# Kernel tuning notes

Measured on AMD Instinct MI355X. Metric: run time of the kernel, lower is better.

## Reference

```python
import jax, jax.numpy as jnp
import numpy as np

DIM = 1024


def _combine(e1, e2):
    # associative op for h_t = a_t * h_{t-1} + b_t (inclusive scan, h_0-contrib handled outside)
    a1, b1 = e1
    a2, b2 = e2
    return a1 * a2, b2 + a2 * b1


def setup_inputs() -> dict:
    key = jax.random.key(0)
    ks = jax.random.split(key, 11)
    s = 1.0 / np.sqrt(DIM)
    d = {
        "x": jax.random.normal(ks[0], (4, 4096, DIM), jnp.float32),
        "hidden": jax.random.normal(ks[1], (4, DIM), jnp.float32),
        "Wf": jax.random.uniform(ks[2], (DIM, DIM), jnp.float32, -s, s),
        "bf": jax.random.uniform(ks[3], (DIM,), jnp.float32, -s, s),
        "Wi": jax.random.uniform(ks[4], (DIM, DIM), jnp.float32, -s, s),
        "bi": jax.random.uniform(ks[5], (DIM,), jnp.float32, -s, s),
        "Wig": jax.random.uniform(ks[6], (DIM, DIM), jnp.float32, -s, s),
        "big": jax.random.uniform(ks[7], (DIM,), jnp.float32, -s, s),
        "Wog": jax.random.uniform(ks[8], (DIM, DIM), jnp.float32, -s, s),
        "bog": jax.random.uniform(ks[9], (DIM,), jnp.float32, -s, s),
    }
    return d


def reference(x, hidden, Wf, bf, Wi, bi, Wig, big, Wog, bog):
    # x: [B, L, D], hidden: [B, D]
    forget = jax.nn.sigmoid(jnp.einsum("bld,ed->ble", x, Wf) + bf)
    inp = jnp.tanh(jnp.einsum("bld,ed->ble", x, Wi) + bi) * \
          jax.nn.sigmoid(jnp.einsum("bld,ed->ble", x, Wig) + big)
    # parallel scan of h_t = forget_t * h_{t-1} + inp_t with h_0 = 0
    _, h_inner = jax.lax.associative_scan(_combine, (forget, inp), axis=1)
    # add initial-hidden contribution: hidden * prod_{s<=t} forget_s
    h = h_inner + hidden[:, None, :] * jnp.cumprod(forget, axis=1)
    y = jnp.tanh(h) * jax.nn.sigmoid(jnp.einsum("bld,ed->ble", x, Wog) + bog)
    return y, h[:, -1, :]
```

## Files before the change

### kernel.cpp

```cpp
#include <hip/hip_runtime.h>
#include <hip/hip_bf16.h>
#include <cstdint>
#include <cstddef>

#define DIMD 1024
#define LSEQ 4096
#define BATCH 4
#define MTOT (BATCH*LSEQ)
#define NCHUNK 64
#define CHUNKLEN 64
#define GATE_ELEMS ((size_t)MTOT*DIMD)
#define NTILE_K 16

typedef __bf16 bf16x8 __attribute__((ext_vector_type(8)));
typedef float f32x4 __attribute__((ext_vector_type(4)));

__device__ __forceinline__ unsigned short f2bf(float f) {
    union { float f; uint32_t u; } v; v.f = f;
    uint32_t r = v.u + 0x7fffu + ((v.u >> 16) & 1u);
    return (unsigned short)(r >> 16);
}
__device__ __forceinline__ float bits2f(unsigned short b) {
    union { uint32_t u; float f; } v; v.u = ((uint32_t)b) << 16; return v.f;
}
__device__ __forceinline__ float gld(const float* p, size_t o) { return p[o]; }
__device__ __forceinline__ float gld(const unsigned short* p, size_t o) { return bits2f(p[o]); }
__device__ __forceinline__ void  gst(float* p, size_t o, float v) { p[o] = v; }
__device__ __forceinline__ void  gst(unsigned short* p, size_t o, float v) { p[o] = f2bf(v); }

__device__ __forceinline__ float fsig(float x) {
    return __builtin_amdgcn_rcpf(1.f + __expf(-x));
}

__global__ void cast_f32_to_bf16(const float* __restrict__ src,
                                 unsigned short* __restrict__ dst, int n) {
    int i = (blockIdx.x * blockDim.x + threadIdx.x) * 8;
    if (i >= n) return;
    float4 a = *(const float4*)(src + i);
    float4 b = *(const float4*)(src + i + 4);
    uint4 o;
    o.x = (uint32_t)f2bf(a.x) | ((uint32_t)f2bf(a.y) << 16);
    o.y = (uint32_t)f2bf(a.z) | ((uint32_t)f2bf(a.w) << 16);
    o.z = (uint32_t)f2bf(b.x) | ((uint32_t)f2bf(b.y) << 16);
    o.w = (uint32_t)f2bf(b.z) | ((uint32_t)f2bf(b.w) << 16);
    *(uint4*)(dst + i) = o;
}

template <typename T>
__global__ __launch_bounds__(512, 1) void gemm_gates8(
    const unsigned short* __restrict__ Xb,
    const unsigned short* __restrict__ Wcat,
    const float* __restrict__ bf_, const float* __restrict__ bi_,
    const float* __restrict__ big_, const float* __restrict__ bog_,
    T* __restrict__ G)
{
    __shared__ __align__(16) char lds[131072];
    char* ldsA = lds;
    char* ldsB = lds + 65536;

    const int tid = threadIdx.x;
    const int wave = tid >> 6, lane = tid & 63;
    const int wm = wave >> 2, wn = wave & 3;
    const int l15 = lane & 15, l4 = lane >> 4;

    const int wg = blockIdx.x;
    const int swz = (wg & 7) * 128 + (wg >> 3);
    const int mt = swz & 63, nt = swz >> 6;
    const int m0 = mt * 256, n0 = nt * 256;

    auto stage = [&](const unsigned short* src, int rowbase, int k0, char* region, int buf) {
#pragma unroll
        for (int half = 0; half < 2; ++half) {
            char* slot = region + (buf * 2 + half) * 16384;
#pragma unroll
            for (int j = 0; j < 2; ++j) {
                int r = (tid >> 3) + j * 64;
                int scol = (tid & 7) ^ (r & 7);
                const unsigned short* g = src + (size_t)(rowbase + half * 128 + r) * DIMD + k0 + scol * 8;
                __builtin_amdgcn_global_load_lds(
                    (const __attribute__((address_space(1))) uint32_t*)g,
                    (__attribute__((address_space(3))) uint32_t*)(slot + (wave << 10) + (j << 13)),
                    16, 0, 0);
            }
        }
    };

    f32x4 acc[8][4];
#pragma unroll
    for (int m = 0; m < 8; ++m)
#pragma unroll
        for (int n = 0; n < 4; ++n) acc[m][n] = (f32x4)0.f;

    stage(Xb, m0, 0, ldsA, 0);   stage(Wcat, n0, 0, ldsB, 0);
    stage(Xb, m0, 64, ldsA, 1);  stage(Wcat, n0, 64, ldsB, 1);

#pragma unroll 1
    for (int t = 0; t < NTILE_K; ++t) {
        const int buf = t & 1;
        if (t == NTILE_K - 1) asm volatile("s_waitcnt vmcnt(0)" ::: "memory");
        else                  asm volatile("s_waitcnt vmcnt(8)" ::: "memory");
        __builtin_amdgcn_s_barrier();

        const char* Aslot = ldsA + (buf * 2 + wm) * 16384;
        const char* Bslot = ldsB + (buf * 2 + (wn >> 1)) * 16384;
        const int rbB = (wn & 1) * 64;

        auto rdA = [&](int mq, int i, int kk) -> bf16x8 {
            int r = (mq * 4 + i) * 16 + l15;
            int s = kk * 4 + l4;
            return *(const bf16x8*)(Aslot + r * 128 + ((s ^ (r & 7)) << 4));
        };
        auto rdB = [&](int nq, int i2, int kk) -> bf16x8 {
            int r = rbB + (nq * 2 + i2) * 16 + l15;
            int s = kk * 4 + l4;
            return *(const bf16x8*)(Bslot + r * 128 + ((s ^ (r & 7)) << 4));
        };

        bf16x8 av0[4][2], av1[4][2], bv0[2][2], bv1[2][2];
#pragma unroll
        for (int i = 0; i < 4; ++i)
#pragma unroll
            for (int kk = 0; kk < 2; ++kk) av0[i][kk] = rdA(0, i, kk);
#pragma unroll
        for (int i2 = 0; i2 < 2; ++i2)
#pragma unroll
            for (int kk = 0; kk < 2; ++kk) { bv0[i2][kk] = rdB(0, i2, kk); bv1[i2][kk] = rdB(1, i2, kk); }

        __builtin_amdgcn_s_setprio(1);
#pragma unroll
        for (int kk = 0; kk < 2; ++kk)
#pragma unroll
            for (int i = 0; i < 4; ++i)
#pragma unroll
                for (int i2 = 0; i2 < 2; ++i2)
                    acc[i][i2] = __builtin_amdgcn_mfma_f32_16x16x32_bf16(av0[i][kk], bv0[i2][kk], acc[i][i2], 0, 0, 0);
        __builtin_amdgcn_s_setprio(0);

#pragma unroll
        for (int i = 0; i < 4; ++i)
#pragma unroll
            for (int kk = 0; kk < 2; ++kk) av1[i][kk] = rdA(1, i, kk);

        __builtin_amdgcn_s_setprio(1);
#pragma unroll
        for (int kk = 0; kk < 2; ++kk)
#pragma unroll
            for (int i = 0; i < 4; ++i)
#pragma unroll
                for (int i2 = 0; i2 < 2; ++i2)
                    acc[i][2 + i2] = __builtin_amdgcn_mfma_f32_16x16x32_bf16(av0[i][kk], bv1[i2][kk], acc[i][2 + i2], 0, 0, 0);
        __builtin_amdgcn_s_setprio(0);

        __builtin_amdgcn_s_setprio(1);
#pragma unroll
        for (int kk = 0; kk < 2; ++kk)
#pragma unroll
            for (int i = 0; i < 4; ++i)
#pragma unroll
                for (int i2 = 0; i2 < 2; ++i2)
                    acc[4 + i][i2] = __builtin_amdgcn_mfma_f32_16x16x32_bf16(av1[i][kk], bv0[i2][kk], acc[4 + i][i2], 0, 0, 0);
        __builtin_amdgcn_s_setprio(0);

        __builtin_amdgcn_s_setprio(1);
#pragma unroll
        for (int kk = 0; kk < 2; ++kk)
#pragma unroll
            for (int i = 0; i < 4; ++i)
#pragma unroll
                for (int i2 = 0; i2 < 2; ++i2)
                    acc[4 + i][2 + i2] = __builtin_amdgcn_mfma_f32_16x16x32_bf16(av1[i][kk], bv1[i2][kk], acc[4 + i][2 + i2], 0, 0, 0);
        __builtin_amdgcn_s_setprio(0);

        __builtin_amdgcn_s_barrier();
        if (t + 2 < NTILE_K) {
            stage(Xb, m0, (t + 2) * 64, ldsA, buf);
            stage(Wcat, n0, (t + 2) * 64, ldsB, buf);
        }
    }

    const int gate = n0 >> 10;
    const float* bias = (gate == 0) ? bf_ : (gate == 1) ? bi_ : (gate == 2) ? big_ : bog_;
    T* Gg = G + (size_t)gate * GATE_ELEMS;
    const int ebase = (n0 & 1023) + wn * 64;
    const int rowb0 = m0 + wm * 128;
    float bvv[4];
#pragma unroll
    for (int nf = 0; nf < 4; ++nf) bvv[nf] = bias[ebase + nf * 16 + l15];
#pragma unroll
    for (int mf = 0; mf < 8; ++mf) {
        int rowb = rowb0 + mf * 16 + l4 * 4;
#pragma unroll
        for (int r = 0; r < 4; ++r) {
            size_t rowoff = (size_t)(rowb + r) * DIMD;
#pragma unroll
            for (int nf = 0; nf < 4; ++nf) {
                float pre = acc[mf][nf][r] + bvv[nf];
                float v = (gate == 1) ? (2.f * fsig(2.f * pre) - 1.f) : fsig(pre);
                gst(Gg, rowoff + ebase + nf * 16 + l15, v);
            }
        }
    }
}

template <typename T>
__global__ void scan_phase1(const T* __restrict__ F, const T* __restrict__ TI,
                            const T* __restrict__ SG,
                            float* __restrict__ Aagg, float* __restrict__ Bagg) {
    const int d = blockIdx.x * blockDim.x + threadIdx.x;
    const int c = blockIdx.y, b = blockIdx.z;
    size_t base = ((size_t)b * LSEQ + (size_t)c * CHUNKLEN) * DIMD + d;
    float A = 1.f, Bv = 0.f;
#pragma unroll 8
    for (int t = 0; t < CHUNKLEN; ++t) {
        size_t off = base + (size_t)t * DIMD;
        float f = gld(F, off);
        float i = gld(TI, off) * gld(SG, off);
        A *= f;
        Bv = __builtin_fmaf(f, Bv, i);
    }
    size_t o = ((size_t)b * NCHUNK + c) * DIMD + d;
    Aagg[o] = A;
    Bagg[o] = Bv;
}

__global__ void scan_phase2(const float* __restrict__ Aagg, const float* __restrict__ Bagg,
                            const float* __restrict__ hidden,
                            float* __restrict__ Hstart, float* __restrict__ out_h) {
    int idx = blockIdx.x * blockDim.x + threadIdx.x;
    int b = idx >> 10, d = idx & 1023;
    float h = hidden[b * 1024 + d];
    for (int c = 0; c < NCHUNK; ++c) {
        size_t o = ((size_t)b * NCHUNK + c) * DIMD + d;
        Hstart[o] = h;
        h = __builtin_fmaf(Aagg[o], h, Bagg[o]);
    }
    out_h[b * 1024 + d] = h;
}

template <typename T>
__global__ void scan_phase3(const T* __restrict__ F, const T* __restrict__ TI,
                            const T* __restrict__ SG, const T* __restrict__ OG,
                            const float* __restrict__ Hstart, float* __restrict__ y) {
    const int d = blockIdx.x * blockDim.x + threadIdx.x;
    const int c = blockIdx.y, b = blockIdx.z;
    float h = Hstart[((size_t)b * NCHUNK + c) * DIMD + d];
    size_t base = ((size_t)b * LSEQ + (size_t)c * CHUNKLEN) * DIMD + d;
#pragma unroll 4
    for (int t = 0; t < CHUNKLEN; ++t) {
        size_t off = base + (size_t)t * DIMD;
        float f = gld(F, off);
        float i = gld(TI, off) * gld(SG, off);
        h = __builtin_fmaf(f, h, i);
        y[off] = tanhf(h) * gld(OG, off);
    }
}

extern "C" void kernel_launch(void* const* d_in, const int* in_sizes, int n_in,
                              void* d_out, int out_size, void* d_ws, size_t ws_size,
                              hipStream_t stream) {
    const float* x      = (const float*)d_in[0];
    const float* hidden = (const float*)d_in[1];
    const float* Wf  = (const float*)d_in[2];
    const float* bf_ = (const float*)d_in[3];
    const float* Wi  = (const float*)d_in[4];
    const float* bi_ = (const float*)d_in[5];
    const float* Wig = (const float*)d_in[6];
    const float* big_= (const float*)d_in[7];
    const float* Wog = (const float*)d_in[8];
    const float* bog_= (const float*)d_in[9];

    char* ws = (char*)d_ws;
    unsigned short* Xb   = (unsigned short*)(ws);
    unsigned short* Wcat = (unsigned short*)(ws + 33554432);

    float* y     = (float*)d_out;
    float* out_h = y + GATE_ELEMS;

    cast_f32_to_bf16<<<MTOT * DIMD / 8 / 256, 256, 0, stream>>>(x, Xb, MTOT * DIMD);
    cast_f32_to_bf16<<<DIMD * DIMD / 8 / 256, 256, 0, stream>>>(Wf,  Wcat + 0 * DIMD * DIMD, DIMD * DIMD);
    cast_f32_to_bf16<<<DIMD * DIMD / 8 / 256, 256, 0, stream>>>(Wi,  Wcat + 1 * DIMD * DIMD, DIMD * DIMD);
    cast_f32_to_bf16<<<DIMD * DIMD / 8 / 256, 256, 0, stream>>>(Wig, Wcat + 2 * DIMD * DIMD, DIMD * DIMD);
    cast_f32_to_bf16<<<DIMD * DIMD / 8 / 256, 256, 0, stream>>>(Wog, Wcat + 3 * DIMD * DIMD, DIMD * DIMD);

    const size_t FP32_WS_NEED = 33554432ull + 8388608ull + GATE_ELEMS * 4 * 4 + 3ull * 1048576ull;
    if (ws_size >= FP32_WS_NEED) {
        float* G      = (float*)(ws + 41943040);
        float* Aagg   = (float*)(ws + 310378496);
        float* Bagg   = (float*)(ws + 311427072);
        float* Hstart = (float*)(ws + 312475648);
        gemm_gates8<float><<<dim3(MTOT / 256 * (4096 / 256)), 512, 0, stream>>>(
            Xb, Wcat, bf_, bi_, big_, bog_, G);
        const float* Fg  = G;
        const float* TIg = G + 1 * GATE_ELEMS;
        const float* SGg = G + 2 * GATE_ELEMS;
        const float* OGg = G + 3 * GATE_ELEMS;
        scan_phase1<float><<<dim3(DIMD / 256, NCHUNK, BATCH), 256, 0, stream>>>(Fg, TIg, SGg, Aagg, Bagg);
        scan_phase2<<<BATCH * DIMD / 256, 256, 0, stream>>>(Aagg, Bagg, hidden, Hstart, out_h);
        scan_phase3<float><<<dim3(DIMD / 256, NCHUNK, BATCH), 256, 0, stream>>>(Fg, TIg, SGg, OGg, Hstart, y);
    } else {
        unsigned short* G = (unsigned short*)(ws + 41943040);
        float* Aagg   = (float*)(ws + 176160768);
        float* Bagg   = (float*)(ws + 177209344);
        float* Hstart = (float*)(ws + 178257920);
        gemm_gates8<unsigned short><<<dim3(MTOT / 256 * (4096 / 256)), 512, 0, stream>>>(
            Xb, Wcat, bf_, bi_, big_, bog_, G);
        const unsigned short* Fg  = G;
        const unsigned short* TIg = G + 1 * GATE_ELEMS;
        const unsigned short* SGg = G + 2 * GATE_ELEMS;
        const unsigned short* OGg = G + 3 * GATE_ELEMS;
        scan_phase1<unsigned short><<<dim3(DIMD / 256, NCHUNK, BATCH), 256, 0, stream>>>(Fg, TIg, SGg, Aagg, Bagg);
        scan_phase2<<<BATCH * DIMD / 256, 256, 0, stream>>>(Aagg, Bagg, hidden, Hstart, out_h);
        scan_phase3<unsigned short><<<dim3(DIMD / 256, NCHUNK, BATCH), 256, 0, stream>>>(Fg, TIg, SGg, OGg, Hstart, y);
    }
}
```

Before: 249.6 us.

## Interleave LDS reads and next-tile prefetch between MFMA clusters in gate GEMM

Restructures the GEMM main loop into four MFMA phases separated by barriers and sched_barriers. LDS fragment reads and the global-to-LDS prefetch of tile t+2 are spread between these phases instead of sitting at the start and end of each iteration. LDS and global address computation moves out of the loop into precomputed base pointers, incremented pointers and a toggled buffer offset. The aim is to overlap memory traffic with matrix-core work and cut per-iteration address arithmetic, at the cost of extra workgroup barriers per K tile.

```diff
diff --git a/kernel.cpp b/kernel.cpp
--- a/kernel.cpp
+++ b/kernel.cpp
@@ -62,11 +62,17 @@
     const int wave = tid >> 6, lane = tid & 63;
     const int wm = wave >> 2, wn = wave & 3;
     const int l15 = lane & 15, l4 = lane >> 4;
+    const int m7 = l15 & 7;
 
     const int wg = blockIdx.x;
     const int swz = (wg & 7) * 128 + (wg >> 3);
     const int mt = swz & 63, nt = swz >> 6;
     const int m0 = mt * 256, n0 = nt * 256;
+
+    const char* Abase0 = ldsA + wm * 16384 + l15 * 128 + (((0 + l4) ^ m7) << 4);
+    const char* Abase1 = ldsA + wm * 16384 + l15 * 128 + (((4 + l4) ^ m7) << 4);
+    const char* Bbase0 = ldsB + (wn >> 1) * 16384 + ((wn & 1) * 64 + l15) * 128 + (((0 + l4) ^ m7) << 4);
+    const char* Bbase1 = ldsB + (wn >> 1) * 16384 + ((wn & 1) * 64 + l15) * 128 + (((4 + l4) ^ m7) << 4);
 
     auto stage = [&](const unsigned short* src, int rowbase, int k0, char* region, int buf) {
 #pragma unroll
@@ -85,6 +91,18 @@
         }
     };
 
+    const unsigned short* pA[2][2];
+    const unsigned short* pB[2][2];
+#pragma unroll
+    for (int half = 0; half < 2; ++half)
+#pragma unroll
+        for (int j = 0; j < 2; ++j) {
+            int r = (tid >> 3) + j * 64;
+            int scol = (tid & 7) ^ (r & 7);
+            pA[half][j] = Xb + (size_t)(m0 + half * 128 + r) * DIMD + 128 + scol * 8;
+            pB[half][j] = Wcat + (size_t)(n0 + half * 128 + r) * DIMD + 128 + scol * 8;
+        }
+
     f32x4 acc[8][4];
 #pragma unroll
     for (int m = 0; m < 8; ++m)
@@ -94,38 +112,28 @@
     stage(Xb, m0, 0, ldsA, 0);   stage(Wcat, n0, 0, ldsB, 0);
     stage(Xb, m0, 64, ldsA, 1);  stage(Wcat, n0, 64, ldsB, 1);
 
+    int bufOff = 0;
 #pragma unroll 1
     for (int t = 0; t < NTILE_K; ++t) {
-        const int buf = t & 1;
         if (t == NTILE_K - 1) asm volatile("s_waitcnt vmcnt(0)" ::: "memory");
         else                  asm volatile("s_waitcnt vmcnt(8)" ::: "memory");
         __builtin_amdgcn_s_barrier();
-
-        const char* Aslot = ldsA + (buf * 2 + wm) * 16384;
-        const char* Bslot = ldsB + (buf * 2 + (wn >> 1)) * 16384;
-        const int rbB = (wn & 1) * 64;
-
-        auto rdA = [&](int mq, int i, int kk) -> bf16x8 {
-            int r = (mq * 4 + i) * 16 + l15;
-            int s = kk * 4 + l4;
-            return *(const bf16x8*)(Aslot + r * 128 + ((s ^ (r & 7)) << 4));
-        };
-        auto rdB = [&](int nq, int i2, int kk) -> bf16x8 {
-            int r = rbB + (nq * 2 + i2) * 16 + l15;
-            int s = kk * 4 + l4;
-            return *(const bf16x8*)(Bslot + r * 128 + ((s ^ (r & 7)) << 4));
-        };
+        __builtin_amdgcn_sched_barrier(0);
 
         bf16x8 av0[4][2], av1[4][2], bv0[2][2], bv1[2][2];
-#pragma unroll
-        for (int i = 0; i < 4; ++i)
-#pragma unroll
-            for (int kk = 0; kk < 2; ++kk) av0[i][kk] = rdA(0, i, kk);
-#pragma unroll
-        for (int i2 = 0; i2 < 2; ++i2)
-#pragma unroll
-            for (int kk = 0; kk < 2; ++kk) { bv0[i2][kk] = rdB(0, i2, kk); bv1[i2][kk] = rdB(1, i2, kk); }
-
+
+#pragma unroll
+        for (int i = 0; i < 4; ++i) {
+            av0[i][0] = *(const bf16x8*)(Abase0 + bufOff + i * 2048);
+            av0[i][1] = *(const bf16x8*)(Abase1 + bufOff + i * 2048);
+        }
+#pragma unroll
+        for (int i2 = 0; i2 < 2; ++i2) {
+            bv0[i2][0] = *(const bf16x8*)(Bbase0 + bufOff + i2 * 2048);
+            bv0[i2][1] = *(const bf16x8*)(Bbase1 + bufOff + i2 * 2048);
+        }
+        __builtin_amdgcn_sched_barrier(0);
+        __builtin_amdgcn_s_barrier();
         __builtin_amdgcn_s_setprio(1);
 #pragma unroll
         for (int kk = 0; kk < 2; ++kk)
@@ -135,12 +143,16 @@
                 for (int i2 = 0; i2 < 2; ++i2)
                     acc[i][i2] = __builtin_amdgcn_mfma_f32_16x16x32_bf16(av0[i][kk], bv0[i2][kk], acc[i][i2], 0, 0, 0);
         __builtin_amdgcn_s_setprio(0);
-
-#pragma unroll
-        for (int i = 0; i < 4; ++i)
-#pragma unroll
-            for (int kk = 0; kk < 2; ++kk) av1[i][kk] = rdA(1, i, kk);
-
+        __builtin_amdgcn_s_barrier();
+        __builtin_amdgcn_sched_barrier(0);
+
+#pragma unroll
+        for (int i2 = 0; i2 < 2; ++i2) {
+            bv1[i2][0] = *(const bf16x8*)(Bbase0 + bufOff + (2 + i2) * 2048);
+            bv1[i2][1] = *(const bf16x8*)(Bbase1 + bufOff + (2 + i2) * 2048);
+        }
+        __builtin_amdgcn_sched_barrier(0);
+        __builtin_amdgcn_s_barrier();
         __builtin_amdgcn_s_setprio(1);
 #pragma unroll
         for (int kk = 0; kk < 2; ++kk)
@@ -150,7 +162,16 @@
                 for (int i2 = 0; i2 < 2; ++i2)
                     acc[i][2 + i2] = __builtin_amdgcn_mfma_f32_16x16x32_bf16(av0[i][kk], bv1[i2][kk], acc[i][2 + i2], 0, 0, 0);
         __builtin_amdgcn_s_setprio(0);
-
+        __builtin_amdgcn_s_barrier();
+        __builtin_amdgcn_sched_barrier(0);
+
+#pragma unroll
+        for (int i = 0; i < 4; ++i) {
+            av1[i][0] = *(const bf16x8*)(Abase0 + bufOff + (4 + i) * 2048);
+            av1[i][1] = *(const bf16x8*)(Abase1 + bufOff + (4 + i) * 2048);
+        }
+        __builtin_amdgcn_sched_barrier(0);
+        __builtin_amdgcn_s_barrier();
         __builtin_amdgcn_s_setprio(1);
 #pragma unroll
         for (int kk = 0; kk < 2; ++kk)
@@ -160,7 +181,33 @@
                 for (int i2 = 0; i2 < 2; ++i2)
                     acc[4 + i][i2] = __builtin_amdgcn_mfma_f32_16x16x32_bf16(av1[i][kk], bv0[i2][kk], acc[4 + i][i2], 0, 0, 0);
         __builtin_amdgcn_s_setprio(0);
-
+        __builtin_amdgcn_s_barrier();
+        __builtin_amdgcn_sched_barrier(0);
+
+        if (t + 2 < NTILE_K) {
+#pragma unroll
+            for (int half = 0; half < 2; ++half)
+#pragma unroll
+                for (int j = 0; j < 2; ++j) {
+                    __builtin_amdgcn_global_load_lds(
+                        (const __attribute__((address_space(1))) uint32_t*)pA[half][j],
+                        (__attribute__((address_space(3))) uint32_t*)(ldsA + bufOff + half * 16384 + (wave << 10) + (j << 13)),
+                        16, 0, 0);
+                    pA[half][j] += 64;
+                }
+#pragma unroll
+            for (int half = 0; half < 2; ++half)
+#pragma unroll
+                for (int j = 0; j < 2; ++j) {
+                    __builtin_amdgcn_global_load_lds(
+                        (const __attribute__((address_space(1))) uint32_t*)pB[half][j],
+                        (__attribute__((address_space(3))) uint32_t*)(ldsB + bufOff + half * 16384 + (wave << 10) + (j << 13)),
+                        16, 0, 0);
+                    pB[half][j] += 64;
+                }
+        }
+        __builtin_amdgcn_sched_barrier(0);
+        __builtin_amdgcn_s_barrier();
         __builtin_amdgcn_s_setprio(1);
 #pragma unroll
         for (int kk = 0; kk < 2; ++kk)
@@ -170,12 +217,10 @@
                 for (int i2 = 0; i2 < 2; ++i2)
                     acc[4 + i][2 + i2] = __builtin_amdgcn_mfma_f32_16x16x32_bf16(av1[i][kk], bv1[i2][kk], acc[4 + i][2 + i2], 0, 0, 0);
         __builtin_amdgcn_s_setprio(0);
-
-        __builtin_amdgcn_s_barrier();
-        if (t + 2 < NTILE_K) {
-            stage(Xb, m0, (t + 2) * 64, ldsA, buf);
-            stage(Wcat, n0, (t + 2) * 64, ldsB, buf);
-        }
+        __builtin_amdgcn_s_barrier();
+        __builtin_amdgcn_sched_barrier(0);
+
+        bufOff ^= 32768;
     }
 
     const int gate = n0 >> 10;
```

New measurement: 257.6 us. 3.2% more time.
